# Performance work log

Measured on AMD Instinct MI355X. Metric: run time of the kernel, lower is better.

The kernel has to match this reference:

```python
import jax, jax.numpy as jnp
import numpy as np

B, T = 256, 128
EMBED, HIDDEN, VOCAB, FC_IN = 256, 512, 1004, 2048


def setup_inputs() -> dict:
    key = jax.random.key(0)
    ks = jax.random.split(key, 12)
    s = 0.02  # init scale
    return {
        "images": jax.random.normal(ks[0], (B, FC_IN), jnp.float32),   # pooled resnet feats
        "captions": jax.random.normal(ks[1], (B, T, HIDDEN), jnp.float32),
        "W_fc": jax.random.normal(ks[2], (EMBED, FC_IN), jnp.float32) * s,
        "b_fc": jax.random.normal(ks[3], (EMBED,), jnp.float32) * s,
        "W_att": jax.random.normal(ks[4], (EMBED, HIDDEN + EMBED), jnp.float32) * s,
        "b_att": jax.random.normal(ks[5], (EMBED,), jnp.float32) * s,
        "W_ih": jax.random.normal(ks[6], (4 * HIDDEN, 2 * EMBED), jnp.float32) * s,
        "b_ih": jax.random.normal(ks[7], (4 * HIDDEN,), jnp.float32) * s,
        "W_hh": jax.random.normal(ks[8], (4 * HIDDEN, HIDDEN), jnp.float32) * s,
        "b_hh": jax.random.normal(ks[9], (4 * HIDDEN,), jnp.float32) * s,
        "W_out": jax.random.normal(ks[10], (VOCAB, HIDDEN), jnp.float32) * s,
        "b_out": jax.random.normal(ks[11], (VOCAB,), jnp.float32) * s,
    }


def reference(images, captions, W_fc, b_fc, W_att, b_att,
              W_ih, b_ih, W_hh, b_hh, W_out, b_out):
    # encoder fc: pooled resnet features -> embed_size
    feats = images @ W_fc.T + b_fc                      # [B, 256]
    b = feats.shape[0]
    h0 = jnp.zeros((b, HIDDEN), feats.dtype)
    c0 = jnp.zeros((b, HIDDEN), feats.dtype)

    def step(carry, emb_t):
        h, c = carry
        # attention over (features, current caption embed)
        ctx = jnp.concatenate([feats, emb_t], axis=-1) @ W_att.T + b_att   # [B, 256]
        x = jnp.concatenate([feats, ctx], axis=-1)                         # [B, 512]
        gates = x @ W_ih.T + b_ih + h @ W_hh.T + b_hh                      # [B, 2048]
        i, f, g, o = jnp.split(gates, 4, axis=-1)                          # torch gate order
        c = jax.nn.sigmoid(f) * c + jax.nn.sigmoid(i) * jnp.tanh(g)
        h = jax.nn.sigmoid(o) * jnp.tanh(c)
        return (h, c), h

    _, hs = jax.lax.scan(step, (h0, c0), jnp.swapaxes(captions, 0, 1))  # hs: [T, B, 512]
    hiddens = jnp.swapaxes(hs, 0, 1)                                    # [B, T, 512]
    return hiddens @ W_out.T + b_out                                    # [B, T, 1004]
```

## Files before the change

kernel.cpp:

```cpp
#include <hip/hip_runtime.h>

#define Tt  128
#define HID 512

__global__ __launch_bounds__(256)
void gemm_bt(const float* __restrict__ A, const float* __restrict__ Bw,
             const float* __restrict__ bias, const float* __restrict__ C0,
             float* __restrict__ C,
             int M, int N, int K, int lda, int ldb, int ldc, int ldc0,
             int c0div, int nperm)
{
    __shared__ float As[16][68];
    __shared__ float Bs[16][68];
    const int n0 = blockIdx.x * 64;
    const int m0 = blockIdx.y * 64;
    const int tid = threadIdx.x;
    const int tx = tid & 15, ty = tid >> 4;
    float acc[4][4];
#pragma unroll
    for (int i = 0; i < 4; i++)
#pragma unroll
        for (int j = 0; j < 4; j++) acc[i][j] = 0.f;

    for (int k0 = 0; k0 < K; k0 += 16) {
#pragma unroll
        for (int i = 0; i < 4; i++) {
            int e = tid + i * 256;
            int m = e >> 4, k = e & 15;
            As[k][m] = A[(size_t)(m0 + m) * lda + (k0 + k)];
        }
#pragma unroll
        for (int i = 0; i < 4; i++) {
            int e = tid + i * 256;
            int n = e >> 4, k = e & 15;
            int gn = n0 + n;
            int gr = nperm ? ((gn & 3) * HID + (gn >> 2)) : gn;
            Bs[k][n] = (gn < N) ? Bw[(size_t)gr * ldb + (k0 + k)] : 0.f;
        }
        __syncthreads();
#pragma unroll
        for (int kk = 0; kk < 16; kk++) {
            float4 av = *(const float4*)&As[kk][ty * 4];
            float4 bv = *(const float4*)&Bs[kk][tx * 4];
            float a[4] = {av.x, av.y, av.z, av.w};
            float b[4] = {bv.x, bv.y, bv.z, bv.w};
#pragma unroll
            for (int i = 0; i < 4; i++)
#pragma unroll
                for (int j = 0; j < 4; j++)
                    acc[i][j] += a[i] * b[j];
        }
        __syncthreads();
    }
#pragma unroll
    for (int i = 0; i < 4; i++) {
        int m = m0 + ty * 4 + i;
        const float* c0row = C0 ? (C0 + (size_t)(m / c0div) * ldc0) : nullptr;
#pragma unroll
        for (int j = 0; j < 4; j++) {
            int n = n0 + tx * 4 + j;
            if (n < N) {
                float v = acc[i][j];
                if (bias)  v += bias[nperm ? ((n & 3) * HID + (n >> 2)) : n];
                if (c0row) v += c0row[n];
                C[(size_t)m * ldc + n] = v;
            }
        }
    }
}

__global__ __launch_bounds__(512, 2)
void lstm_seq(const float* __restrict__ gin, const float* __restrict__ Whh,
              float* __restrict__ hA, float* __restrict__ hB,
              float* __restrict__ hiddens, unsigned int* __restrict__ flags)
{
    __shared__ float4 Hs[4096];
    const int tid = threadIdx.x;
    const int l   = tid & 63;
    const int w   = tid >> 6;
    const int bt  = blockIdx.x & 7;
    const int jt  = blockIdx.x >> 3;
    const int b0  = bt * 32;
    const int j0  = jt * 16;
    const int ot  = l >> 5;
    const int kc  = l & 31;

    float4 Wr[8][4];
#pragma unroll
    for (int r = 0; r < 8; ++r) {
        int jj = r >> 2, g = r & 3;
        const float* src = Whh + (size_t)(g * HID + j0 + w * 2 + jj) * HID + kc * 16;
#pragma unroll
        for (int q = 0; q < 4; ++q) Wr[r][q] = *(const float4*)(src + q * 4);
    }

    const int ip  = kc >> 2;
    const int jjp = (kc >> 1) & 1;
    const int gH  = kc & 1;
    const int bp  = b0 + ot * 16 + gH * 8 + ip;
    const int jp  = j0 + w * 2 + jjp;
    const size_t hpos = ((size_t)bp * 128 + ((jp >> 2) & 3) * 32 + (jp >> 4)) * 4 + (jp & 3);

    float cr = 0.f;

    for (int t = 0; t < Tt; ++t) {
        float4 gv = *(const float4*)(gin + ((size_t)bp * Tt + t) * 2048 + jp * 4);

        float rA0 = 0.f, rA1 = 0.f, rB0 = 0.f, rB1 = 0.f;
        if (t > 0) {
            if (tid == 0) {
                while (__hip_atomic_load(&flags[bt], __ATOMIC_ACQUIRE,
                                         __HIP_MEMORY_SCOPE_AGENT) < 32u * (unsigned)t)
                    __builtin_amdgcn_s_sleep(1);
            }
            __syncthreads();
            {
                const float4* hin4 =
                    (const float4*)(((t - 1) & 1) ? hB : hA) + (size_t)b0 * 128;
                float4 tmp[8];
#pragma unroll
                for (int q = 0; q < 8; ++q)
                    tmp[q] = hin4[(q * 8 + w) * 64 + l];
#pragma unroll
                for (int q = 0; q < 8; ++q)
                    Hs[(q * 8 + w) * 64 + l] = tmp[q];
            }
            __syncthreads();

#pragma unroll
            for (int hb = 0; hb < 2; ++hb) {
                float P[64];
#pragma unroll
                for (int v = 0; v < 64; ++v) P[v] = 0.f;
#pragma unroll
                for (int i = 0; i < 8; ++i) {
                    const float4* hp = &Hs[(ot * 16 + hb * 8 + i) * 128 + kc];
                    float4 h0 = hp[0], h1 = hp[32], h2 = hp[64], h3 = hp[96];
#pragma unroll
                    for (int r = 0; r < 8; ++r) {
                        P[i * 8 + r] +=
                            Wr[r][0].x * h0.x + Wr[r][0].y * h0.y + Wr[r][0].z * h0.z + Wr[r][0].w * h0.w +
                            Wr[r][1].x * h1.x + Wr[r][1].y * h1.y + Wr[r][1].z * h1.z + Wr[r][1].w * h1.w +
                            Wr[r][2].x * h2.x + Wr[r][2].y * h2.y + Wr[r][2].z * h2.z + Wr[r][2].w * h2.w +
                            Wr[r][3].x * h3.x + Wr[r][3].y * h3.y + Wr[r][3].z * h3.z + Wr[r][3].w * h3.w;
                    }
                }
#define RS_STEP(MASK, CNT)                                              \
                {                                                       \
                    const int Hh = (CNT) / 2;                           \
                    const bool hi = (l & (MASK)) != 0;                  \
                    _Pragma("unroll")                                   \
                    for (int x = 0; x < Hh; ++x) {                      \
                        float a = P[x], b2 = P[Hh + x];                 \
                        float keep = hi ? b2 : a;                       \
                        float send = hi ? a : b2;                       \
                        P[x] = keep + __shfl_xor(send, (MASK), 64);     \
                    }                                                   \
                }
                RS_STEP(16, 64)
                RS_STEP(8, 32)
                RS_STEP(4, 16)
                RS_STEP(2, 8)
                RS_STEP(1, 4)
#undef RS_STEP
                if (hb == 0) { rA0 = P[0]; rA1 = P[1]; }
                else         { rB0 = P[0]; rB1 = P[1]; }
            }
        }
        float own0 = gH ? rB0 : rA0;
        float own1 = gH ? rB1 : rA1;
        float snd0 = gH ? rA0 : rB0;
        float snd1 = gH ? rA1 : rB1;
        float oth0 = __shfl_xor(snd0, 1, 64);
        float oth1 = __shfl_xor(snd1, 1, 64);
        float gi = (gH ? oth0 : own0) + gv.x;
        float gf = (gH ? oth1 : own1) + gv.y;
        float gg = (gH ? own0 : oth0) + gv.z;
        float go = (gH ? own1 : oth1) + gv.w;

        float si = 1.f / (1.f + __expf(-gi));
        float sf = 1.f / (1.f + __expf(-gf));
        float so = 1.f / (1.f + __expf(-go));
        float tg = 1.f - 2.f / (1.f + __expf(2.f * gg));
        float cv = sf * cr + si * tg;
        cr = cv;
        float th = 1.f - 2.f / (1.f + __expf(2.f * cv));
        float hv = so * th;

        float* hw = (t & 1) ? hB : hA;
        hw[hpos] = hv;
        hiddens[((size_t)bp * Tt + t) * HID + jp] = hv;
        __syncthreads();
        if (tid == 0) {
            __threadfence();
            __hip_atomic_fetch_add(&flags[bt], 1u, __ATOMIC_RELEASE,
                                   __HIP_MEMORY_SCOPE_AGENT);
        }
    }
}

extern "C" void kernel_launch(void* const* d_in, const int* in_sizes, int n_in,
                              void* d_out, int out_size, void* d_ws, size_t ws_size,
                              hipStream_t stream)
{
    const float* images = (const float*)d_in[0];
    const float* caps   = (const float*)d_in[1];
    const float* W_fc   = (const float*)d_in[2];
    const float* b_fc   = (const float*)d_in[3];
    const float* W_att  = (const float*)d_in[4];
    const float* b_att  = (const float*)d_in[5];
    const float* W_ih   = (const float*)d_in[6];
    const float* b_ih   = (const float*)d_in[7];
    const float* W_hh   = (const float*)d_in[8];
    const float* b_hh   = (const float*)d_in[9];
    const float* W_out  = (const float*)d_in[10];
    const float* b_out  = (const float*)d_in[11];
    float* out = (float*)d_out;

    float* ws       = (float*)d_ws;
    float* feats    = ws;
    float* att_base = feats + 65536;
    float* gin_base = att_base + 65536;
    float* hA       = gin_base + 524288;
    float* hB       = hA + 131072;
    float* ctx_all  = hB + 131072;
    float* hiddens  = ctx_all + 8388608;
    float* gin_all  = hiddens + 16777216;
    unsigned int* flags = (unsigned int*)(gin_all + 67108864);

    hipMemsetAsync(flags, 0, 8 * sizeof(unsigned int), stream);

    gemm_bt<<<dim3(4, 4), 256, 0, stream>>>(images, W_fc, b_fc, nullptr, feats,
        256, 256, 2048, 2048, 2048, 256, 0, 1, 0);
    gemm_bt<<<dim3(4, 4), 256, 0, stream>>>(feats, W_att, b_att, nullptr, att_base,
        256, 256, 256, 256, 768, 256, 0, 1, 0);
    gemm_bt<<<dim3(32, 4), 256, 0, stream>>>(feats, W_ih, b_ih, nullptr, gin_base,
        256, 2048, 256, 256, 512, 2048, 0, 1, 1);
    gemm_bt<<<dim3(4, 512), 256, 0, stream>>>(caps, W_att + 256, nullptr, att_base, ctx_all,
        32768, 256, 512, 512, 768, 256, 256, Tt, 0);
    gemm_bt<<<dim3(32, 512), 256, 0, stream>>>(ctx_all, W_ih + 256, b_hh, gin_base, gin_all,
        32768, 2048, 256, 256, 512, 2048, 2048, Tt, 1);

    {
        void* args[] = { (void*)&gin_all, (void*)&W_hh, (void*)&hA, (void*)&hB,
                         (void*)&hiddens, (void*)&flags };
        hipLaunchCooperativeKernel((void*)lstm_seq, dim3(256), dim3(512),
                                   args, 0, stream);
    }

    gemm_bt<<<dim3(16, 512), 256, 0, stream>>>(hiddens, W_out, b_out, nullptr, out,
        32768, 1004, 512, 512, 512, 1004, 0, 1, 0);
}
```

Baseline: 6.111 ms.

## Split Whh register tile across half-waves and use DPP for short-distance reductions

Each half-wave now holds only two of the four gates for its two hidden units, so per-lane W_hh registers drop from 32 float4 to 16, and the partial-sum array shrinks from 64 to 32. The batch loop runs four passes of eight rows instead of two passes of sixteen. The xor-1 and xor-2 steps of the reduce-scatter use DPP quad permutes instead of ds_bpermute shuffles. After the loop, two extra cross-half-wave shuffles regather the four gate values per lane. The intent is to relieve register pressure and cut shuffle latency on the serial recurrence, at the cost of more LDS reads of h per step.

```diff
diff --git a/kernel.cpp b/kernel.cpp
--- a/kernel.cpp
+++ b/kernel.cpp
@@ -2,6 +2,12 @@
 
 #define Tt  128
 #define HID 512
+
+#define DPP_QP(x, CTRL) \
+    __int_as_float(__builtin_amdgcn_update_dpp( \
+        __float_as_int(x), __float_as_int(x), (CTRL), 0xF, 0xF, false))
+#define DPP_XOR1(x) DPP_QP(x, 0xB1)
+#define DPP_XOR2(x) DPP_QP(x, 0x4E)
 
 __global__ __launch_bounds__(256)
 void gemm_bt(const float* __restrict__ A, const float* __restrict__ Bw,
@@ -82,23 +88,25 @@
     const int jt  = blockIdx.x >> 3;
     const int b0  = bt * 32;
     const int j0  = jt * 16;
-    const int ot  = l >> 5;
+    const int rh  = l >> 5;
     const int kc  = l & 31;
 
-    float4 Wr[8][4];
-#pragma unroll
-    for (int r = 0; r < 8; ++r) {
-        int jj = r >> 2, g = r & 3;
-        const float* src = Whh + (size_t)(g * HID + j0 + w * 2 + jj) * HID + kc * 16;
-#pragma unroll
-        for (int q = 0; q < 4; ++q) Wr[r][q] = *(const float4*)(src + q * 4);
-    }
-
-    const int ip  = kc >> 2;
-    const int jjp = (kc >> 1) & 1;
-    const int gH  = kc & 1;
-    const int bp  = b0 + ot * 16 + gH * 8 + ip;
-    const int jp  = j0 + w * 2 + jjp;
+    float4 Wr[4][4];
+#pragma unroll
+    for (int jj = 0; jj < 2; ++jj)
+#pragma unroll
+        for (int gg = 0; gg < 2; ++gg) {
+            const float4* src = (const float4*)Whh +
+                (size_t)((rh * 2 + gg) * HID + j0 + w * 2 + jj) * 128 + kc * 4;
+#pragma unroll
+            for (int q2 = 0; q2 < 4; ++q2) Wr[jj * 2 + gg][q2] = src[q2];
+        }
+
+    const int i_p  = ((kc & 1) << 2) | (kc & 2) | ((kc >> 2) & 1);
+    const int jj_p = (kc >> 3) & 1;
+    const int gg_p = (kc >> 4) & 1;
+    const int bp = b0 + (rh * 2 + gg_p) * 8 + i_p;
+    const int jp = j0 + w * 2 + jj_p;
     const size_t hpos = ((size_t)bp * 128 + ((jp >> 2) & 3) * 32 + (jp >> 4)) * 4 + (jp & 3);
 
     float cr = 0.f;
@@ -106,7 +114,7 @@
     for (int t = 0; t < Tt; ++t) {
         float4 gv = *(const float4*)(gin + ((size_t)bp * Tt + t) * 2048 + jp * 4);
 
-        float rA0 = 0.f, rA1 = 0.f, rB0 = 0.f, rB1 = 0.f;
+        float Xv0 = 0.f, Xv1 = 0.f, Xv2 = 0.f, Xv3 = 0.f;
         if (t > 0) {
             if (tid == 0) {
                 while (__hip_atomic_load(&flags[bt], __ATOMIC_ACQUIRE,
@@ -119,77 +127,114 @@
                     (const float4*)(((t - 1) & 1) ? hB : hA) + (size_t)b0 * 128;
                 float4 tmp[8];
 #pragma unroll
-                for (int q = 0; q < 8; ++q)
-                    tmp[q] = hin4[(q * 8 + w) * 64 + l];
-#pragma unroll
-                for (int q = 0; q < 8; ++q)
-                    Hs[(q * 8 + w) * 64 + l] = tmp[q];
+                for (int q2 = 0; q2 < 8; ++q2)
+                    tmp[q2] = hin4[(q2 * 8 + w) * 64 + l];
+#pragma unroll
+                for (int q2 = 0; q2 < 8; ++q2)
+                    Hs[(q2 * 8 + w) * 64 + l] = tmp[q2];
             }
             __syncthreads();
 
 #pragma unroll
-            for (int hb = 0; hb < 2; ++hb) {
-                float P[64];
-#pragma unroll
-                for (int v = 0; v < 64; ++v) P[v] = 0.f;
+            for (int gb = 0; gb < 4; ++gb) {
+                float P[32];
+#pragma unroll
+                for (int v = 0; v < 32; ++v) P[v] = 0.f;
 #pragma unroll
                 for (int i = 0; i < 8; ++i) {
-                    const float4* hp = &Hs[(ot * 16 + hb * 8 + i) * 128 + kc];
+                    const float4* hp = &Hs[(gb * 8 + i) * 128 + kc];
                     float4 h0 = hp[0], h1 = hp[32], h2 = hp[64], h3 = hp[96];
 #pragma unroll
-                    for (int r = 0; r < 8; ++r) {
-                        P[i * 8 + r] +=
+                    for (int r = 0; r < 4; ++r) {
+                        P[i * 4 + r] +=
                             Wr[r][0].x * h0.x + Wr[r][0].y * h0.y + Wr[r][0].z * h0.z + Wr[r][0].w * h0.w +
                             Wr[r][1].x * h1.x + Wr[r][1].y * h1.y + Wr[r][1].z * h1.z + Wr[r][1].w * h1.w +
                             Wr[r][2].x * h2.x + Wr[r][2].y * h2.y + Wr[r][2].z * h2.z + Wr[r][2].w * h2.w +
                             Wr[r][3].x * h3.x + Wr[r][3].y * h3.y + Wr[r][3].z * h3.z + Wr[r][3].w * h3.w;
                     }
                 }
-#define RS_STEP(MASK, CNT)                                              \
-                {                                                       \
-                    const int Hh = (CNT) / 2;                           \
-                    const bool hi = (l & (MASK)) != 0;                  \
-                    _Pragma("unroll")                                   \
-                    for (int x = 0; x < Hh; ++x) {                      \
-                        float a = P[x], b2 = P[Hh + x];                 \
-                        float keep = hi ? b2 : a;                       \
-                        float send = hi ? a : b2;                       \
-                        P[x] = keep + __shfl_xor(send, (MASK), 64);     \
-                    }                                                   \
-                }
-                RS_STEP(16, 64)
-                RS_STEP(8, 32)
-                RS_STEP(4, 16)
-                RS_STEP(2, 8)
-                RS_STEP(1, 4)
-#undef RS_STEP
-                if (hb == 0) { rA0 = P[0]; rA1 = P[1]; }
-                else         { rB0 = P[0]; rB1 = P[1]; }
-            }
-        }
-        float own0 = gH ? rB0 : rA0;
-        float own1 = gH ? rB1 : rA1;
-        float snd0 = gH ? rA0 : rB0;
-        float snd1 = gH ? rA1 : rB1;
-        float oth0 = __shfl_xor(snd0, 1, 64);
-        float oth1 = __shfl_xor(snd1, 1, 64);
-        float gi = (gH ? oth0 : own0) + gv.x;
-        float gf = (gH ? oth1 : own1) + gv.y;
-        float gg = (gH ? own0 : oth0) + gv.z;
-        float go = (gH ? own1 : oth1) + gv.w;
-
-        float si = 1.f / (1.f + __expf(-gi));
-        float sf = 1.f / (1.f + __expf(-gf));
-        float so = 1.f / (1.f + __expf(-go));
-        float tg = 1.f - 2.f / (1.f + __expf(2.f * gg));
-        float cv = sf * cr + si * tg;
-        cr = cv;
-        float th = 1.f - 2.f / (1.f + __expf(2.f * cv));
-        float hv = so * th;
-
-        float* hw = (t & 1) ? hB : hA;
-        hw[hpos] = hv;
-        hiddens[((size_t)bp * Tt + t) * HID + jp] = hv;
+                {
+                    const bool hi = (l & 1) != 0;
+#pragma unroll
+                    for (int x = 0; x < 16; ++x) {
+                        float a = P[x], b2 = P[16 + x];
+                        float keep = hi ? b2 : a;
+                        float send = hi ? a : b2;
+                        P[x] = keep + DPP_XOR1(send);
+                    }
+                }
+                {
+                    const bool hi = (l & 2) != 0;
+#pragma unroll
+                    for (int x = 0; x < 8; ++x) {
+                        float a = P[x], b2 = P[8 + x];
+                        float keep = hi ? b2 : a;
+                        float send = hi ? a : b2;
+                        P[x] = keep + DPP_XOR2(send);
+                    }
+                }
+                {
+                    const bool hi = (l & 4) != 0;
+#pragma unroll
+                    for (int x = 0; x < 4; ++x) {
+                        float a = P[x], b2 = P[4 + x];
+                        float keep = hi ? b2 : a;
+                        float send = hi ? a : b2;
+                        P[x] = keep + __shfl_xor(send, 4, 64);
+                    }
+                }
+                {
+                    const bool hi = (l & 8) != 0;
+#pragma unroll
+                    for (int x = 0; x < 2; ++x) {
+                        float a = P[x], b2 = P[2 + x];
+                        float keep = hi ? b2 : a;
+                        float send = hi ? a : b2;
+                        P[x] = keep + __shfl_xor(send, 8, 64);
+                    }
+                }
+                {
+                    const bool hi = (l & 16) != 0;
+                    float a = P[0], b2 = P[1];
+                    float keep = hi ? b2 : a;
+                    float send = hi ? a : b2;
+                    P[0] = keep + __shfl_xor(send, 16, 64);
+                }
+                if      (gb == 0) Xv0 = P[0];
+                else if (gb == 1) Xv1 = P[0];
+                else if (gb == 2) Xv2 = P[0];
+                else              Xv3 = P[0];
+            }
+        }
+        {
+            const bool qb = rh != 0, pb = gg_p != 0;
+            float rA = __shfl_xor(qb ? Xv0 : Xv2, 32, 64);
+            float rB = __shfl_xor(qb ? Xv1 : Xv3, 32, 64);
+            float U0 = qb ? rA : Xv0, U1 = qb ? rB : Xv1;
+            float U2 = qb ? Xv2 : rA, U3 = qb ? Xv3 : rB;
+            float sA = __shfl_xor(pb ? U0 : U1, 16, 64);
+            float sB = __shfl_xor(pb ? U2 : U3, 16, 64);
+            float Y0 = pb ? sA : U0, Y1 = pb ? U1 : sA;
+            float Y2 = pb ? sB : U2, Y3 = pb ? U3 : sB;
+
+            float gi = Y0 + gv.x;
+            float gf = Y1 + gv.y;
+            float gc = Y2 + gv.z;
+            float go = Y3 + gv.w;
+
+            float si = 1.f / (1.f + __expf(-gi));
+            float sf = 1.f / (1.f + __expf(-gf));
+            float so = 1.f / (1.f + __expf(-go));
+            float tg = 1.f - 2.f / (1.f + __expf(2.f * gc));
+            float cv = sf * cr + si * tg;
+            cr = cv;
+            float th = 1.f - 2.f / (1.f + __expf(2.f * cv));
+            float hv = so * th;
+
+            float* hw = (t & 1) ? hB : hA;
+            hw[hpos] = hv;
+            hiddens[((size_t)bp * Tt + t) * HID + jp] = hv;
+        }
         __syncthreads();
         if (tid == 0) {
             __threadfence();
```

New measurement: 7.274 ms. 19.0% more time.
